# Kernel optimization log

Hardware: AMD Instinct MI355X
Metric: run time of the kernel (lower is better)

The kernel has to match this reference:

```python
import jax, jax.numpy as jnp
import numpy as np

TAU = 1.0      # temperature for gumbel-softmax
EPS = 1e-12    # F.normalize eps


def _l2norm(v, axis):
    n = jnp.sqrt(jnp.sum(v * v, axis=axis, keepdims=True))
    return v / jnp.maximum(n, EPS)


def setup_inputs() -> dict:
    key = jax.random.key(0)
    k1, k2, k3, k4 = jax.random.split(key, 4)
    b, c, h, w, n = 8, 512, 64, 64, 1024
    x = jax.random.normal(k1, (b, c, h, w), dtype=jnp.float32)
    centers = jax.random.normal(k2, (n, c), dtype=jnp.float32)          # VQ codebook
    clusters = jax.random.normal(k3, (n, c), dtype=jnp.float32)         # ClusterLookup param
    gumbel_noise = jax.random.gumbel(k4, (b, n, h, w), dtype=jnp.float32)
    return {"x": x, "centers": centers, "clusters": clusters, "gumbel_noise": gumbel_noise}


def reference(x, centers, clusters, gumbel_noise):
    # similarity logits: [b, n, h, w]
    inner = jnp.einsum('bchw,nc->bnhw', x, centers)
    # hard gumbel-softmax (straight-through) over code dim
    y_soft = jax.nn.softmax((inner + gumbel_noise) / TAU, axis=1)
    idx = jnp.argmax(y_soft, axis=1)                                     # [b, h, w]
    y_hard = jax.nn.one_hot(idx, centers.shape[0], axis=1, dtype=y_soft.dtype)
    one_hot = y_hard - jax.lax.stop_gradient(y_soft) + y_soft            # [b, n, h, w]
    # quantized features: codebook lookup expressed as einsum
    z_q = jnp.einsum('bnhw,nd->bdhw', one_hot, centers)                  # [b, c, h, w]
    # ClusterLookup(z_q, alpha=None, is_direct=False)
    nf = _l2norm(z_q, axis=1)
    ncl = _l2norm(clusters, axis=1)
    ip = jnp.einsum('bchw,nc->bnhw', nf, ncl)                            # cluster logits
    preds = jnp.argmax(ip, axis=1)                                       # [b, h, w] int
    probs = jax.nn.one_hot(preds, clusters.shape[0], axis=1, dtype=ip.dtype)
    cluster_loss = -jnp.mean(jnp.sum(probs * ip, axis=1))
    return (cluster_loss, preds, ip, z_q)
```

## Files before the change

kernel.cpp:

```cpp
#include <hip/hip_runtime.h>
#include <math.h>

#define C 512
#define HW 4096
#define N 1024
#define NPIX 32768
#define MARGIN 2.0f
#define CAP 512

typedef short s16x8 __attribute__((ext_vector_type(8)));
typedef float f32x4 __attribute__((ext_vector_type(4)));

__device__ inline unsigned short f2bf(float f) {
    unsigned int u = __float_as_uint(f);
    return (unsigned short)((u + 0x7FFFu + ((u >> 16) & 1u)) >> 16);
}
__device__ inline float h2f(unsigned short u) {
    _Float16 h; __builtin_memcpy(&h, &u, 2); return (float)h;
}
__device__ inline unsigned short f2h(float f) {
    _Float16 h = (_Float16)f; unsigned short u; __builtin_memcpy(&u, &h, 2); return u;
}
__device__ inline unsigned int mono(float v) {
    unsigned int u = __float_as_uint(v);
    return (u & 0x80000000u) ? ~u : (u | 0x80000000u);
}
__device__ inline float unmono(unsigned int u) {
    unsigned int v = (u & 0x80000000u) ? (u & 0x7FFFFFFFu) : ~u;
    return __uint_as_float(v);
}
__device__ inline int xsw(int px, int G) { return px * 512 + ((G ^ (px & 7)) << 2); }

__global__ __launch_bounds__(64) void k_norms(const float* __restrict__ centers,
                                              const float* __restrict__ clusters,
                                              float* __restrict__ cnorm,
                                              float* __restrict__ clnorm) {
    int r = blockIdx.x;
    const float* src = (r < N) ? (centers + (size_t)r * C) : (clusters + (size_t)(r - N) * C);
    int lane = threadIdx.x;
    float s = 0.f;
    for (int k = lane; k < C; k += 64) { float v = src[k]; s += v * v; }
    #pragma unroll
    for (int m = 1; m < 64; m <<= 1) s += __shfl_xor(s, m, 64);
    if (lane == 0) {
        float nrm = sqrtf(s);
        if (nrm < 1e-12f) nrm = 1e-12f;
        if (r < N) cnorm[r] = nrm; else clnorm[r - N] = nrm;
    }
}

__global__ __launch_bounds__(256) void k_gemmM(const float* __restrict__ centers,
                                               const float* __restrict__ clusters,
                                               const float* __restrict__ cnorm,
                                               const float* __restrict__ clnorm,
                                               float* __restrict__ M) {
    __shared__ float as[32][68];
    __shared__ float bs[32][68];
    int tid = threadIdx.x;
    int tx = tid & 15, ty = tid >> 4;
    int i0 = blockIdx.x * 64, j0 = blockIdx.y * 64;
    int lrow = tid >> 2, lkq = (tid & 3) * 8;
    float acc[4][4] = {};
    for (int kc = 0; kc < C; kc += 32) {
        float4 a0 = *(const float4*)(centers + (size_t)(i0 + lrow) * C + kc + lkq);
        float4 a1 = *(const float4*)(centers + (size_t)(i0 + lrow) * C + kc + lkq + 4);
        float4 b0 = *(const float4*)(clusters + (size_t)(j0 + lrow) * C + kc + lkq);
        float4 b1 = *(const float4*)(clusters + (size_t)(j0 + lrow) * C + kc + lkq + 4);
        __syncthreads();
        as[lkq+0][lrow]=a0.x; as[lkq+1][lrow]=a0.y; as[lkq+2][lrow]=a0.z; as[lkq+3][lrow]=a0.w;
        as[lkq+4][lrow]=a1.x; as[lkq+5][lrow]=a1.y; as[lkq+6][lrow]=a1.z; as[lkq+7][lrow]=a1.w;
        bs[lkq+0][lrow]=b0.x; bs[lkq+1][lrow]=b0.y; bs[lkq+2][lrow]=b0.z; bs[lkq+3][lrow]=b0.w;
        bs[lkq+4][lrow]=b1.x; bs[lkq+5][lrow]=b1.y; bs[lkq+6][lrow]=b1.z; bs[lkq+7][lrow]=b1.w;
        __syncthreads();
        #pragma unroll
        for (int k = 0; k < 32; k += 4) {
            float av[4][4], bv[4][4];
            #pragma unroll
            for (int kk = 0; kk < 4; ++kk) {
                float4 ta = *(const float4*)&as[k+kk][tx*4];
                float4 tb = *(const float4*)&bs[k+kk][ty*4];
                av[kk][0]=ta.x; av[kk][1]=ta.y; av[kk][2]=ta.z; av[kk][3]=ta.w;
                bv[kk][0]=tb.x; bv[kk][1]=tb.y; bv[kk][2]=tb.z; bv[kk][3]=tb.w;
            }
            #pragma unroll
            for (int kk = 0; kk < 4; ++kk)
                #pragma unroll
                for (int ii = 0; ii < 4; ++ii)
                    #pragma unroll
                    for (int jj = 0; jj < 4; ++jj)
                        acc[ii][jj] = fmaf(av[kk][ii], bv[kk][jj], acc[ii][jj]);
        }
    }
    float rci[4], rcj[4];
    #pragma unroll
    for (int ii = 0; ii < 4; ++ii) rci[ii] = cnorm[i0 + tx*4 + ii];
    #pragma unroll
    for (int jj = 0; jj < 4; ++jj) rcj[jj] = clnorm[j0 + ty*4 + jj];
    #pragma unroll
    for (int ii = 0; ii < 4; ++ii)
        #pragma unroll
        for (int jj = 0; jj < 4; ++jj)
            M[(size_t)(i0 + tx*4 + ii) * N + (j0 + ty*4 + jj)] = acc[ii][jj] / (rci[ii] * rcj[jj]);
}

__global__ __launch_bounds__(256) void k_rowstat(const float* __restrict__ M,
                                                 float* __restrict__ rowmax,
                                                 int* __restrict__ rowarg) {
    __shared__ float sv[256];
    __shared__ int   sa[256];
    int i = blockIdx.x, tid = threadIdx.x;
    float bv = -INFINITY; int ba = 0;
    for (int j = tid; j < N; j += 256) {
        float v = M[(size_t)i * N + j];
        if (v > bv || (v == bv && j < ba)) { bv = v; ba = j; }
    }
    sv[tid] = bv; sa[tid] = ba;
    __syncthreads();
    for (int s = 128; s > 0; s >>= 1) {
        if (tid < s) {
            float v = sv[tid + s]; int a = sa[tid + s];
            if (v > sv[tid] || (v == sv[tid] && a < sa[tid])) { sv[tid] = v; sa[tid] = a; }
        }
        __syncthreads();
    }
    if (tid == 0) { rowmax[i] = sv[0]; rowarg[i] = sa[0]; }
}

__global__ __launch_bounds__(64) void k_cenfrag(const float* __restrict__ centers,
                                                unsigned short* __restrict__ cenB) {
    int f = blockIdx.x;
    int nt = f >> 4, kt = f & 15;
    int lane = threadIdx.x;
    int r = lane & 15, g = lane >> 4;
    const float* src = centers + (size_t)(nt * 16 + r) * C + kt * 32 + g * 4;
    float4 lo = *(const float4*)src;
    float4 hi = *(const float4*)(src + 16);
    union { unsigned short us[8]; uint4 q; } u;
    u.us[0]=f2bf(lo.x); u.us[1]=f2bf(lo.y); u.us[2]=f2bf(lo.z); u.us[3]=f2bf(lo.w);
    u.us[4]=f2bf(hi.x); u.us[5]=f2bf(hi.y); u.us[6]=f2bf(hi.z); u.us[7]=f2bf(hi.w);
    *(uint4*)(cenB + ((size_t)f * 64 + lane) * 8) = u.q;
}

__global__ __launch_bounds__(256, 3) void k_fused(const float* __restrict__ x,
                                                  const unsigned short* __restrict__ cenB,
                                                  const float* __restrict__ gumbel,
                                                  const float* __restrict__ centers,
                                                  int* __restrict__ idxb) {
    __shared__ float xs[C * 16];
    __shared__ unsigned int pmax[16];
    __shared__ unsigned long long pixkey[16];
    __shared__ unsigned int candlist[CAP];
    __shared__ int candcount;

    int tid = threadIdx.x;
    int lane = tid & 63, w = tid >> 6;
    int r = lane & 15, g = lane >> 4;

    int tile = (int)((blockIdx.x >> 3) | ((blockIdx.x & 7) << 8));
    int p0 = tile << 4;
    int b = p0 >> 12, hw0 = p0 & (HW - 1);

    if (tid < 16) { pmax[tid] = 0u; pixkey[tid] = 0ull; }
    if (tid == 0) candcount = 0;

    const float* xb = x + (size_t)b * C * HW + hw0;
    {
        int k0 = tid >> 2, q = (tid & 3) << 2;
        #pragma unroll
        for (int kk = 0; kk < 8; ++kk) {
            int k = kk * 64 + k0;
            float4 v = *(const float4*)(xb + (size_t)k * HW + q);
            int G = k >> 2, e = k & 3;
            xs[xsw(q + 0, G) + e] = v.x;
            xs[xsw(q + 1, G) + e] = v.y;
            xs[xsw(q + 2, G) + e] = v.z;
            xs[xsw(q + 3, G) + e] = v.w;
        }
    }
    __syncthreads();

    s16x8 a[16];
    #pragma unroll
    for (int kt = 0; kt < 16; ++kt) {
        float4 lo = *(const float4*)&xs[xsw(r, kt * 8 + g)];
        float4 hi = *(const float4*)&xs[xsw(r, kt * 8 + g + 4)];
        s16x8 t;
        t[0] = (short)f2bf(lo.x); t[1] = (short)f2bf(lo.y);
        t[2] = (short)f2bf(lo.z); t[3] = (short)f2bf(lo.w);
        t[4] = (short)f2bf(hi.x); t[5] = (short)f2bf(hi.y);
        t[6] = (short)f2bf(hi.z); t[7] = (short)f2bf(hi.w);
        a[kt] = t;
    }

    unsigned int keepH[32];
    float m4[4] = {-INFINITY, -INFINITY, -INFINITY, -INFINITY};
    const float* grow = gumbel + ((size_t)b * N + r) * HW + hw0 + g * 4;
    #pragma unroll
    for (int nt = 0; nt < 16; ++nt) {
        int ntg = (w << 4) + nt;
        const unsigned short* bp = cenB + (size_t)ntg * 16 * 512 + lane * 8;
        float4 gv = *(const float4*)(grow + (size_t)ntg * 16 * HW);
        f32x4 acc0 = {0.f, 0.f, 0.f, 0.f};
        f32x4 acc1 = {0.f, 0.f, 0.f, 0.f};
        #pragma unroll
        for (int kt = 0; kt < 16; kt += 2) {
            s16x8 b0 = *(const s16x8*)(bp + (size_t)kt * 512);
            s16x8 b1 = *(const s16x8*)(bp + (size_t)(kt + 1) * 512);
            acc0 = __builtin_amdgcn_mfma_f32_16x16x32_bf16(a[kt],     b0, acc0, 0, 0, 0);
            acc1 = __builtin_amdgcn_mfma_f32_16x16x32_bf16(a[kt + 1], b1, acc1, 0, 0, 0);
        }
        float v0 = acc0[0] + acc1[0] + gv.x;
        float v1 = acc0[1] + acc1[1] + gv.y;
        float v2 = acc0[2] + acc1[2] + gv.z;
        float v3 = acc0[3] + acc1[3] + gv.w;
        m4[0] = fmaxf(m4[0], v0); m4[1] = fmaxf(m4[1], v1);
        m4[2] = fmaxf(m4[2], v2); m4[3] = fmaxf(m4[3], v3);
        keepH[nt * 2]     = (unsigned int)f2h(v0) | ((unsigned int)f2h(v1) << 16);
        keepH[nt * 2 + 1] = (unsigned int)f2h(v2) | ((unsigned int)f2h(v3) << 16);
    }

    #pragma unroll
    for (int s2 = 1; s2 < 16; s2 <<= 1)
        #pragma unroll
        for (int j = 0; j < 4; ++j) m4[j] = fmaxf(m4[j], __shfl_xor(m4[j], s2, 64));
    if (r == 0) {
        #pragma unroll
        for (int j = 0; j < 4; ++j) atomicMax(&pmax[g * 4 + j], mono(m4[j]));
    }
    __syncthreads();

    float thr[4];
    #pragma unroll
    for (int j = 0; j < 4; ++j) thr[j] = unmono(pmax[g * 4 + j]) - MARGIN;
    #pragma unroll
    for (int nt = 0; nt < 16; ++nt) {
        int n0 = (((w << 4) + nt) << 4) + r;
        #pragma unroll
        for (int j2 = 0; j2 < 2; ++j2) {
            unsigned int pk = keepH[nt * 2 + j2];
            float lo = h2f((unsigned short)(pk & 0xFFFFu));
            float hi = h2f((unsigned short)(pk >> 16));
            int j = j2 * 2;
            if (lo >= thr[j]) {
                int pos = atomicAdd(&candcount, 1);
                if (pos < CAP) candlist[pos] = (unsigned int)n0 | ((unsigned int)(g * 4 + j) << 12);
            }
            if (hi >= thr[j + 1]) {
                int pos = atomicAdd(&candcount, 1);
                if (pos < CAP) candlist[pos] = (unsigned int)n0 | ((unsigned int)(g * 4 + j + 1) << 12);
            }
        }
    }
    __syncthreads();

    int cc = candcount; if (cc > CAP) cc = CAP;
    int sl = lane & 15, cg = lane >> 4;
    for (int t0 = w * 4; t0 < cc; t0 += 16) {
        int c = t0 + cg;
        bool valid = c < cc;
        unsigned int e = candlist[valid ? c : 0];
        int n = (int)(e & 1023u), pl = (int)(e >> 12);
        const float* cen = centers + (size_t)n * C;
        float s = 0.f;
        #pragma unroll
        for (int m = 0; m < 8; ++m) {
            int G = sl + (m << 4);
            float4 xv = *(const float4*)&xs[xsw(pl, G)];
            float4 cv = *(const float4*)(cen + (G << 2));
            s = fmaf(xv.x, cv.x, s); s = fmaf(xv.y, cv.y, s);
            s = fmaf(xv.z, cv.z, s); s = fmaf(xv.w, cv.w, s);
        }
        #pragma unroll
        for (int s2 = 1; s2 < 16; s2 <<= 1) s += __shfl_xor(s, s2, 64);
        if (valid && sl == 0) {
            float val = s + gumbel[((size_t)b * N + n) * HW + hw0 + pl];
            unsigned long long key = ((unsigned long long)mono(val) << 32) | (unsigned int)(1023 - n);
            atomicMax(&pixkey[pl], key);
        }
    }
    __syncthreads();
    if (tid < 16) idxb[p0 + tid] = 1023 - (int)(unsigned int)(pixkey[tid] & 0xFFFFFFFFull);
}

__global__ __launch_bounds__(256) void k_preds(const int* __restrict__ idxb,
                                               const float* __restrict__ rowmax,
                                               const int* __restrict__ rowarg,
                                               float* __restrict__ preds_out,
                                               float* __restrict__ partial) {
    __shared__ float sv[256];
    int gid = blockIdx.x * 256 + threadIdx.x;
    int i = idxb[gid];
    preds_out[gid] = (float)rowarg[i];
    sv[threadIdx.x] = rowmax[i];
    __syncthreads();
    for (int s = 128; s > 0; s >>= 1) {
        if (threadIdx.x < s) sv[threadIdx.x] += sv[threadIdx.x + s];
        __syncthreads();
    }
    if (threadIdx.x == 0) partial[blockIdx.x] = sv[0];
}

__global__ __launch_bounds__(256) void k_gather(const float* __restrict__ src, int ncols,
                                                const int* __restrict__ idx,
                                                float* __restrict__ dst) {
    __shared__ float rows[64][65];
    int tile = blockIdx.x;
    int col0 = blockIdx.y * 64;
    int tid = threadIdx.x;
    int lane = tid & 63, w = tid >> 6;
    int b = tile >> 6, hw0 = (tile & 63) << 6;
    #pragma unroll
    for (int r8 = 0; r8 < 16; ++r8) {
        int r = w * 16 + r8;
        int row = idx[tile * 64 + r];
        rows[r][lane] = src[(size_t)row * ncols + col0 + lane];
    }
    __syncthreads();
    #pragma unroll
    for (int jj = 0; jj < 16; ++jj) {
        int j = col0 + w * 16 + jj;
        dst[((size_t)b * ncols + j) * HW + hw0 + lane] = rows[lane][w * 16 + jj];
    }
}

__global__ __launch_bounds__(128) void k_loss(const float* __restrict__ partial,
                                              float* __restrict__ out) {
    __shared__ float sv[128];
    sv[threadIdx.x] = partial[threadIdx.x];
    __syncthreads();
    for (int s = 64; s > 0; s >>= 1) {
        if (threadIdx.x < s) sv[threadIdx.x] += sv[threadIdx.x + s];
        __syncthreads();
    }
    if (threadIdx.x == 0) out[0] = -(sv[0] / 32768.0f);
}

extern "C" void kernel_launch(void* const* d_in, const int* in_sizes, int n_in,
                              void* d_out, int out_size, void* d_ws, size_t ws_size,
                              hipStream_t stream) {
    const float* x        = (const float*)d_in[0];
    const float* centers  = (const float*)d_in[1];
    const float* clusters = (const float*)d_in[2];
    const float* gumbel   = (const float*)d_in[3];
    float* out = (float*)d_out;

    char* w = (char*)d_ws;
    int*   idxb    = (int*)w;
    float* cnorm   = (float*)(w + 131072);
    float* clnorm  = cnorm + 1024;
    float* rowmax  = clnorm + 1024;
    int*   rowarg  = (int*)(rowmax + 1024);
    float* partial = (float*)(rowarg + 1024);
    float* M       = (float*)(w + 262144);
    unsigned short* cenB = (unsigned short*)(w + 4456448);

    float* out_loss  = out;
    float* out_preds = out + 1;
    float* out_ip    = out + 1 + 32768;
    float* out_zq    = out + 1 + 32768 + (size_t)N * NPIX;

    k_norms  <<<2048, 64, 0, stream>>>(centers, clusters, cnorm, clnorm);
    k_gemmM  <<<dim3(16, 16), 256, 0, stream>>>(centers, clusters, cnorm, clnorm, M);
    k_rowstat<<<1024, 256, 0, stream>>>(M, rowmax, rowarg);
    k_cenfrag<<<1024, 64, 0, stream>>>(centers, cenB);
    k_fused  <<<2048, 256, 0, stream>>>(x, cenB, gumbel, centers, idxb);
    k_preds  <<<128, 256, 0, stream>>>(idxb, rowmax, rowarg, out_preds, partial);
    k_gather <<<dim3(512, 16), 256, 0, stream>>>(M, N, idxb, out_ip);
    k_gather <<<dim3(512, 8),  256, 0, stream>>>(centers, C, idxb, out_zq);
    k_loss   <<<1, 128, 0, stream>>>(partial, out_loss);
}
```

Baseline: 288.2 us.

## Widen fused VQ block to 64 pixels with LDS-staged double-buffered codebook tiles

```diff
diff --git a/kernel.cpp b/kernel.cpp
--- a/kernel.cpp
+++ b/kernel.cpp
@@ -6,7 +6,8 @@
 #define N 1024
 #define NPIX 32768
 #define MARGIN 2.0f
-#define CAP 512
+#define BLKPX 64
+#define WAVES 4
 
 typedef short s16x8 __attribute__((ext_vector_type(8)));
 typedef float f32x4 __attribute__((ext_vector_type(4)));
@@ -25,11 +26,9 @@
     unsigned int u = __float_as_uint(v);
     return (u & 0x80000000u) ? ~u : (u | 0x80000000u);
 }
-__device__ inline float unmono(unsigned int u) {
-    unsigned int v = (u & 0x80000000u) ? (u & 0x7FFFFFFFu) : ~u;
-    return __uint_as_float(v);
-}
-__device__ inline int xsw(int px, int G) { return px * 512 + ((G ^ (px & 7)) << 2); }
+__device__ inline int xsw(int p, int G) {
+    return p * 512 + ((G ^ (((p >> 2) & 7) ^ ((p & 3) << 1))) << 2);
+}
 
 __global__ __launch_bounds__(64) void k_norms(const float* __restrict__ centers,
                                               const float* __restrict__ clusters,
@@ -141,49 +140,58 @@
     *(uint4*)(cenB + ((size_t)f * 64 + lane) * 8) = u.q;
 }
 
-__global__ __launch_bounds__(256, 3) void k_fused(const float* __restrict__ x,
+__global__ __launch_bounds__(256, 1) void k_fused(const float* __restrict__ x,
                                                   const unsigned short* __restrict__ cenB,
                                                   const float* __restrict__ gumbel,
                                                   const float* __restrict__ centers,
                                                   int* __restrict__ idxb) {
-    __shared__ float xs[C * 16];
-    __shared__ unsigned int pmax[16];
-    __shared__ unsigned long long pixkey[16];
-    __shared__ unsigned int candlist[CAP];
-    __shared__ int candcount;
+    __shared__ float xs[BLKPX * 512];
+    __shared__ unsigned short cen[16 * 512];
+    __shared__ unsigned long long pixkey[BLKPX];
+    __shared__ unsigned int candlist[WAVES][256];
+    __shared__ int candcount[WAVES];
 
     int tid = threadIdx.x;
     int lane = tid & 63, w = tid >> 6;
     int r = lane & 15, g = lane >> 4;
 
-    int tile = (int)((blockIdx.x >> 3) | ((blockIdx.x & 7) << 8));
-    int p0 = tile << 4;
+    int p0 = blockIdx.x * BLKPX;
     int b = p0 >> 12, hw0 = p0 & (HW - 1);
 
-    if (tid < 16) { pmax[tid] = 0u; pixkey[tid] = 0ull; }
-    if (tid == 0) candcount = 0;
+    if (tid < BLKPX) pixkey[tid] = 0ull;
+    if (tid < WAVES) candcount[tid] = 0;
+
+    const uint4* cb = (const uint4*)cenB;
+    uint4* cl = (uint4*)cen;
+    #pragma unroll
+    for (int j = 0; j < 4; ++j) cl[j * 256 + tid] = cb[j * 256 + tid];
 
     const float* xb = x + (size_t)b * C * HW + hw0;
     {
-        int k0 = tid >> 2, q = (tid & 3) << 2;
-        #pragma unroll
-        for (int kk = 0; kk < 8; ++kk) {
-            int k = kk * 64 + k0;
-            float4 v = *(const float4*)(xb + (size_t)k * HW + q);
+        int q = tid & 15, k0 = tid >> 4;
+        #pragma unroll
+        for (int kk = 0; kk < 32; ++kk) {
+            int k = kk * 16 + k0;
+            float4 v = *(const float4*)(xb + (size_t)k * HW + q * 4);
             int G = k >> 2, e = k & 3;
-            xs[xsw(q + 0, G) + e] = v.x;
-            xs[xsw(q + 1, G) + e] = v.y;
-            xs[xsw(q + 2, G) + e] = v.z;
-            xs[xsw(q + 3, G) + e] = v.w;
-        }
-    }
-    __syncthreads();
+            xs[xsw(q * 4 + 0, G) + e] = v.x;
+            xs[xsw(q * 4 + 1, G) + e] = v.y;
+            xs[xsw(q * 4 + 2, G) + e] = v.z;
+            xs[xsw(q * 4 + 3, G) + e] = v.w;
+        }
+    }
+    __syncthreads();
+
+    uint4 cr0 = cb[1024 + tid], cr1 = cb[1280 + tid], cr2 = cb[1536 + tid], cr3 = cb[1792 + tid];
+    const float* gbase = gumbel + (size_t)b * N * HW + hw0 + w * 16 + g * 4;
+    float4 gv_c = *(const float4*)(gbase + (size_t)r * HW);
+    float4 gv_n = *(const float4*)(gbase + (size_t)(16 + r) * HW);
 
     s16x8 a[16];
     #pragma unroll
     for (int kt = 0; kt < 16; ++kt) {
-        float4 lo = *(const float4*)&xs[xsw(r, kt * 8 + g)];
-        float4 hi = *(const float4*)&xs[xsw(r, kt * 8 + g + 4)];
+        float4 lo = *(const float4*)&xs[xsw(w * 16 + r, kt * 8 + g)];
+        float4 hi = *(const float4*)&xs[xsw(w * 16 + r, kt * 8 + 4 + g)];
         s16x8 t;
         t[0] = (short)f2bf(lo.x); t[1] = (short)f2bf(lo.y);
         t[2] = (short)f2bf(lo.z); t[3] = (short)f2bf(lo.w);
@@ -192,81 +200,88 @@
         a[kt] = t;
     }
 
-    unsigned int keepH[32];
     float m4[4] = {-INFINITY, -INFINITY, -INFINITY, -INFINITY};
-    const float* grow = gumbel + ((size_t)b * N + r) * HW + hw0 + g * 4;
-    #pragma unroll
-    for (int nt = 0; nt < 16; ++nt) {
-        int ntg = (w << 4) + nt;
-        const unsigned short* bp = cenB + (size_t)ntg * 16 * 512 + lane * 8;
-        float4 gv = *(const float4*)(grow + (size_t)ntg * 16 * HW);
-        f32x4 acc0 = {0.f, 0.f, 0.f, 0.f};
-        f32x4 acc1 = {0.f, 0.f, 0.f, 0.f};
-        #pragma unroll
-        for (int kt = 0; kt < 16; kt += 2) {
-            s16x8 b0 = *(const s16x8*)(bp + (size_t)kt * 512);
-            s16x8 b1 = *(const s16x8*)(bp + (size_t)(kt + 1) * 512);
-            acc0 = __builtin_amdgcn_mfma_f32_16x16x32_bf16(a[kt],     b0, acc0, 0, 0, 0);
-            acc1 = __builtin_amdgcn_mfma_f32_16x16x32_bf16(a[kt + 1], b1, acc1, 0, 0, 0);
-        }
-        float v0 = acc0[0] + acc1[0] + gv.x;
-        float v1 = acc0[1] + acc1[1] + gv.y;
-        float v2 = acc0[2] + acc1[2] + gv.z;
-        float v3 = acc0[3] + acc1[3] + gv.w;
-        m4[0] = fmaxf(m4[0], v0); m4[1] = fmaxf(m4[1], v1);
-        m4[2] = fmaxf(m4[2], v2); m4[3] = fmaxf(m4[3], v3);
-        keepH[nt * 2]     = (unsigned int)f2h(v0) | ((unsigned int)f2h(v1) << 16);
-        keepH[nt * 2 + 1] = (unsigned int)f2h(v2) | ((unsigned int)f2h(v3) << 16);
-    }
-
-    #pragma unroll
-    for (int s2 = 1; s2 < 16; s2 <<= 1)
-        #pragma unroll
-        for (int j = 0; j < 4; ++j) m4[j] = fmaxf(m4[j], __shfl_xor(m4[j], s2, 64));
-    if (r == 0) {
-        #pragma unroll
-        for (int j = 0; j < 4; ++j) atomicMax(&pmax[g * 4 + j], mono(m4[j]));
-    }
-    __syncthreads();
-
-    float thr[4];
-    #pragma unroll
-    for (int j = 0; j < 4; ++j) thr[j] = unmono(pmax[g * 4 + j]) - MARGIN;
-    #pragma unroll
-    for (int nt = 0; nt < 16; ++nt) {
-        int n0 = (((w << 4) + nt) << 4) + r;
-        #pragma unroll
-        for (int j2 = 0; j2 < 2; ++j2) {
-            unsigned int pk = keepH[nt * 2 + j2];
-            float lo = h2f((unsigned short)(pk & 0xFFFFu));
-            float hi = h2f((unsigned short)(pk >> 16));
-            int j = j2 * 2;
-            if (lo >= thr[j]) {
-                int pos = atomicAdd(&candcount, 1);
-                if (pos < CAP) candlist[pos] = (unsigned int)n0 | ((unsigned int)(g * 4 + j) << 12);
+    for (int ntc = 0; ntc < 8; ++ntc) {
+        unsigned int keepH[16];
+        #pragma unroll
+        for (int s = 0; s < 8; ++s) {
+            int nt = ntc * 8 + s;
+            int ntf = (nt + 2 <= 63) ? nt + 2 : 63;
+            float4 gv_f = *(const float4*)(gbase + (size_t)(ntf * 16 + r) * HW);
+            const s16x8* bp = (const s16x8*)cen + lane;
+            f32x4 acc0 = {0.f, 0.f, 0.f, 0.f};
+            f32x4 acc1 = {0.f, 0.f, 0.f, 0.f};
+            #pragma unroll
+            for (int kt = 0; kt < 16; kt += 2) {
+                s16x8 b0 = bp[kt * 64];
+                s16x8 b1 = bp[(kt + 1) * 64];
+                acc0 = __builtin_amdgcn_mfma_f32_16x16x32_bf16(a[kt],     b0, acc0, 0, 0, 0);
+                acc1 = __builtin_amdgcn_mfma_f32_16x16x32_bf16(a[kt + 1], b1, acc1, 0, 0, 0);
             }
-            if (hi >= thr[j + 1]) {
-                int pos = atomicAdd(&candcount, 1);
-                if (pos < CAP) candlist[pos] = (unsigned int)n0 | ((unsigned int)(g * 4 + j + 1) << 12);
+            float v0 = acc0[0] + acc1[0] + gv_c.x;
+            float v1 = acc0[1] + acc1[1] + gv_c.y;
+            float v2 = acc0[2] + acc1[2] + gv_c.z;
+            float v3 = acc0[3] + acc1[3] + gv_c.w;
+            m4[0] = fmaxf(m4[0], v0); m4[1] = fmaxf(m4[1], v1);
+            m4[2] = fmaxf(m4[2], v2); m4[3] = fmaxf(m4[3], v3);
+            keepH[s * 2]     = (unsigned int)f2h(v0) | ((unsigned int)f2h(v1) << 16);
+            keepH[s * 2 + 1] = (unsigned int)f2h(v2) | ((unsigned int)f2h(v3) << 16);
+            __builtin_amdgcn_s_barrier();
+            __builtin_amdgcn_sched_barrier(0);
+            cl[tid] = cr0; cl[256 + tid] = cr1; cl[512 + tid] = cr2; cl[768 + tid] = cr3;
+            {
+                const uint4* src = cb + (size_t)ntf * 1024;
+                cr0 = src[tid]; cr1 = src[256 + tid]; cr2 = src[512 + tid]; cr3 = src[768 + tid];
             }
-        }
-    }
-    __syncthreads();
-
-    int cc = candcount; if (cc > CAP) cc = CAP;
+            asm volatile("s_waitcnt lgkmcnt(0)" ::: "memory");
+            __builtin_amdgcn_s_barrier();
+            __builtin_amdgcn_sched_barrier(0);
+            gv_c = gv_n; gv_n = gv_f;
+        }
+        #pragma unroll
+        for (int s2 = 1; s2 < 16; s2 <<= 1) {
+            #pragma unroll
+            for (int j = 0; j < 4; ++j) m4[j] = fmaxf(m4[j], __shfl_xor(m4[j], s2, 64));
+        }
+        float thr[4];
+        #pragma unroll
+        for (int j = 0; j < 4; ++j) thr[j] = m4[j] - MARGIN;
+        #pragma unroll
+        for (int s = 0; s < 8; ++s) {
+            int nn = (ntc * 8 + s) * 16 + r;
+            #pragma unroll
+            for (int j2 = 0; j2 < 2; ++j2) {
+                unsigned int pk = keepH[s * 2 + j2];
+                float lo = h2f((unsigned short)(pk & 0xFFFFu));
+                float hi = h2f((unsigned short)(pk >> 16));
+                if (lo >= thr[j2 * 2]) {
+                    int pos = atomicAdd(&candcount[w], 1);
+                    if (pos < 256) candlist[w][pos] =
+                        (unsigned int)nn | ((unsigned int)(w * 16 + g * 4 + j2 * 2) << 10);
+                }
+                if (hi >= thr[j2 * 2 + 1]) {
+                    int pos = atomicAdd(&candcount[w], 1);
+                    if (pos < 256) candlist[w][pos] =
+                        (unsigned int)nn | ((unsigned int)(w * 16 + g * 4 + j2 * 2 + 1) << 10);
+                }
+            }
+        }
+    }
+
+    int cc = candcount[w]; if (cc > 256) cc = 256;
     int sl = lane & 15, cg = lane >> 4;
-    for (int t0 = w * 4; t0 < cc; t0 += 16) {
+    for (int t0 = 0; t0 < cc; t0 += 4) {
         int c = t0 + cg;
         bool valid = c < cc;
-        unsigned int e = candlist[valid ? c : 0];
-        int n = (int)(e & 1023u), pl = (int)(e >> 12);
-        const float* cen = centers + (size_t)n * C;
+        unsigned int e = candlist[w][valid ? c : 0];
+        int n = (int)(e & 1023u), pl = (int)(e >> 10);
+        const float* cenr = centers + (size_t)n * C;
         float s = 0.f;
         #pragma unroll
         for (int m = 0; m < 8; ++m) {
             int G = sl + (m << 4);
             float4 xv = *(const float4*)&xs[xsw(pl, G)];
-            float4 cv = *(const float4*)(cen + (G << 2));
+            float4 cv = *(const float4*)(cenr + (G << 2));
             s = fmaf(xv.x, cv.x, s); s = fmaf(xv.y, cv.y, s);
             s = fmaf(xv.z, cv.z, s); s = fmaf(xv.w, cv.w, s);
         }
@@ -279,7 +294,7 @@
         }
     }
     __syncthreads();
-    if (tid < 16) idxb[p0 + tid] = 1023 - (int)(unsigned int)(pixkey[tid] & 0xFFFFFFFFull);
+    if (tid < BLKPX) idxb[p0 + tid] = 1023 - (int)(unsigned int)(pixkey[tid] & 0xFFFFFFFFull);
 }
 
 __global__ __launch_bounds__(256) void k_preds(const int* __restrict__ idxb,
@@ -363,7 +378,7 @@
     k_gemmM  <<<dim3(16, 16), 256, 0, stream>>>(centers, clusters, cnorm, clnorm, M);
     k_rowstat<<<1024, 256, 0, stream>>>(M, rowmax, rowarg);
     k_cenfrag<<<1024, 64, 0, stream>>>(centers, cenB);
-    k_fused  <<<2048, 256, 0, stream>>>(x, cenB, gumbel, centers, idxb);
+    k_fused  <<<512, 256, 0, stream>>>(x, cenB, gumbel, centers, idxb);
     k_preds  <<<128, 256, 0, stream>>>(idxb, rowmax, rowarg, out_preds, partial);
     k_gather <<<dim3(512, 16), 256, 0, stream>>>(M, N, idxb, out_ip);
     k_gather <<<dim3(512, 8),  256, 0, stream>>>(centers, C, idxb, out_zq);
```

Measured after the change: 247.3 us. 14.2% less time.
